# Performance work log

Hardware: AMD Instinct MI355X
Metric: run time of the kernel (lower is better)

Reference implementation:

```python
import jax, jax.numpy as jnp
import numpy as np

N_NODES = 65536
N_EDGES = 524288
N_LAYERS = 3
D = 128
ED = 32
BATCH = 64
NEG_SLOPE = 0.2


def setup_inputs() -> dict:
    key = jax.random.key(0)
    ks = jax.random.split(key, 10)
    w_scale = 1.0 / np.sqrt(D)
    return {
        "x": jax.random.normal(ks[0], (N_NODES, D), dtype=jnp.float32),
        "edge_index": jax.random.randint(ks[1], (2, N_EDGES), 0, N_NODES, dtype=jnp.int32),
        "edge_attr": jax.random.normal(ks[2], (N_EDGES, ED), dtype=jnp.float32),
        "Ws": jax.random.normal(ks[3], (N_LAYERS, D, D), dtype=jnp.float32) * w_scale,
        "att_src": jax.random.normal(ks[4], (N_LAYERS, D), dtype=jnp.float32) * w_scale,
        "att_dst": jax.random.normal(ks[5], (N_LAYERS, D), dtype=jnp.float32) * w_scale,
        "W_edge": jax.random.normal(ks[6], (N_LAYERS, ED, D), dtype=jnp.float32) * (1.0 / np.sqrt(ED)),
        "att_edge": jax.random.normal(ks[7], (N_LAYERS, D), dtype=jnp.float32) * w_scale,
        "bias": jnp.zeros((N_LAYERS, D), dtype=jnp.float32),
        "batch_size": BATCH,
    }


def _gat_layer(x, src, dst, ea, W, a_s, a_d, We, a_e, b, n):
    # PyG GATConv, heads=1, concat=True, flow source_to_target.
    h = x @ W                                      # [N, D]
    al = (h @ a_s)[src] + (h @ a_d)[dst] + (ea @ We) @ a_e   # [E]
    al = jax.nn.leaky_relu(al, NEG_SLOPE)
    # segment softmax over destination-node neighborhoods
    m = jax.ops.segment_max(al, dst, num_segments=n)
    ex = jnp.exp(al - m[dst])
    den = jax.ops.segment_sum(ex, dst, num_segments=n)
    w = ex / den[dst]                              # [E]
    out = jax.ops.segment_sum(w[:, None] * h[src], dst, num_segments=n)
    return out + b


def reference(x, edge_index, edge_attr, Ws, att_src, att_dst, W_edge, att_edge, bias, batch_size):
    n = x.shape[0]
    # add_self_loops with fill_value='mean': self-loop edge_attr is the mean of
    # incoming edge features per destination node (zero if no incoming edges).
    loop = jnp.arange(n, dtype=edge_index.dtype)
    src = jnp.concatenate([edge_index[0], loop])
    dst = jnp.concatenate([edge_index[1], loop])
    cnt = jax.ops.segment_sum(jnp.ones((edge_attr.shape[0],), edge_attr.dtype), edge_index[1], num_segments=n)
    fill = jax.ops.segment_sum(edge_attr, edge_index[1], num_segments=n) / jnp.maximum(cnt, 1.0)[:, None]
    ea = jnp.concatenate([edge_attr, fill], axis=0)

    h = x
    for l in range(Ws.shape[0]):
        h = jax.nn.gelu(
            _gat_layer(h, src, dst, ea, Ws[l], att_src[l], att_dst[l], W_edge[l], att_edge[l], bias[l], n),
            approximate=False,
        )
        # dropout p=0.2 is identity in eval mode
    return h.reshape(batch_size, n // batch_size, -1)
```

## Files before the change

### kernel.cpp

```cpp
#include <hip/hip_runtime.h>
#include <math.h>

#define NN 65536
#define NE 524288
#define D 128
#define ED 32
#define NEG_SLOPE 0.2f

typedef short bf16x8 __attribute__((ext_vector_type(8)));
typedef float f32x4 __attribute__((ext_vector_type(4)));
typedef unsigned short ushort_t;

__device__ __forceinline__ float leaky(float x) { return x > 0.f ? x : NEG_SLOPE * x; }
__device__ __forceinline__ float gelu_exact(float x) {
    return 0.5f * x * (1.f + erff(x * 0.70710678118654752440f));
}
__device__ __forceinline__ unsigned short bf16_rne(float x) {
    unsigned u = __float_as_uint(x);
    return (unsigned short)((u + 0x7FFFu + ((u >> 16) & 1u)) >> 16);
}
__device__ __forceinline__ void unpack8(int4 r, float* f) {
    unsigned u0 = (unsigned)r.x, u1 = (unsigned)r.y, u2 = (unsigned)r.z, u3 = (unsigned)r.w;
    f[0] = __uint_as_float(u0 << 16); f[1] = __uint_as_float(u0 & 0xFFFF0000u);
    f[2] = __uint_as_float(u1 << 16); f[3] = __uint_as_float(u1 & 0xFFFF0000u);
    f[4] = __uint_as_float(u2 << 16); f[5] = __uint_as_float(u2 & 0xFFFF0000u);
    f[6] = __uint_as_float(u3 << 16); f[7] = __uint_as_float(u3 & 0xFFFF0000u);
}


__global__ void k_wvec(const float* __restrict__ We, const float* __restrict__ ae, float* __restrict__ wvec) {
    int t = threadIdx.x;
    if (t < 3 * ED) {
        int l = t / ED, k = t % ED;
        const float* w = We + (long)(l * ED + k) * D;
        const float* a = ae + (long)l * D;
        float s = 0.f;
        #pragma unroll
        for (int i = 0; i < D; ++i) s += w[i] * a[i];
        wvec[t] = s;
    }
}

__global__ void k_ale_hist(const float* __restrict__ ea, const float* __restrict__ wvec,
                           const int* __restrict__ dstArr, int* __restrict__ deg,
                           float* __restrict__ ale0, float* __restrict__ ale1,
                           float* __restrict__ ale2) {
    int e = blockIdx.x * 256 + threadIdx.x;
    atomicAdd(&deg[dstArr[e]], 1);
    const float4* row = (const float4*)(ea + (long)e * ED);
    const float4* w0 = (const float4*)(wvec);
    const float4* w1 = (const float4*)(wvec + ED);
    const float4* w2 = (const float4*)(wvec + 2 * ED);
    float s0 = 0.f, s1 = 0.f, s2 = 0.f;
    #pragma unroll
    for (int i = 0; i < ED / 4; ++i) {
        float4 v = row[i];
        float4 a = w0[i], b = w1[i], c = w2[i];
        s0 += v.x * a.x + v.y * a.y + v.z * a.z + v.w * a.w;
        s1 += v.x * b.x + v.y * b.y + v.z * b.z + v.w * b.w;
        s2 += v.x * c.x + v.y * c.y + v.z * c.z + v.w * c.w;
    }
    ale0[e] = s0;
    ale1[e] = s1;
    ale2[e] = s2;
}

__global__ void k_scan1(const int* __restrict__ deg, int* __restrict__ rp, int* __restrict__ bsum) {
    __shared__ int s[256];
    int t = threadIdx.x;
    int i = blockIdx.x * 256 + t;
    int v = deg[i];
    s[t] = v;
    __syncthreads();
    #pragma unroll
    for (int off = 1; off < 256; off <<= 1) {
        int x = (t >= off) ? s[t - off] : 0;
        __syncthreads();
        s[t] += x;
        __syncthreads();
    }
    rp[i] = s[t] - v;
    if (t == 255) bsum[blockIdx.x] = s[t];
}

__global__ void k_scan2(const int* __restrict__ bsum, int* __restrict__ bscan, int* __restrict__ rp) {
    __shared__ int s[256];
    int t = threadIdx.x;
    int v = bsum[t];
    s[t] = v;
    __syncthreads();
    #pragma unroll
    for (int off = 1; off < 256; off <<= 1) {
        int x = (t >= off) ? s[t - off] : 0;
        __syncthreads();
        s[t] += x;
        __syncthreads();
    }
    bscan[t] = s[t] - v;
    if (t == 255) rp[NN] = s[t];
}

__global__ void k_scan3(int* __restrict__ rp, const int* __restrict__ bscan, int* __restrict__ cursor) {
    int i = blockIdx.x * 256 + threadIdx.x;
    int v = rp[i] + bscan[blockIdx.x];
    rp[i] = v;
    cursor[i] = v;
}

__global__ void k_scatter4(const int* __restrict__ srcArr, const int* __restrict__ dstArr,
                           int* __restrict__ cursor, const float* __restrict__ ale0,
                           const float* __restrict__ ale1, const float* __restrict__ ale2,
                           int4* __restrict__ edata) {
    int base = blockIdx.x * 1024 + threadIdx.x;
    int e[4], d[4], p[4];
    #pragma unroll
    for (int i = 0; i < 4; ++i) e[i] = base + 256 * i;
    #pragma unroll
    for (int i = 0; i < 4; ++i) d[i] = dstArr[e[i]];
    #pragma unroll
    for (int i = 0; i < 4; ++i) p[i] = atomicAdd(&cursor[d[i]], 1);
    #pragma unroll
    for (int i = 0; i < 4; ++i) {
        edata[p[i]] = make_int4(srcArr[e[i]], __float_as_int(ale0[e[i]]),
                                __float_as_int(ale1[e[i]]), __float_as_int(ale2[e[i]]));
    }
}

__global__ void k_wpack(const float* __restrict__ Ws, short* __restrict__ Whp, short* __restrict__ Wlp) {
    int t = blockIdx.x * 256 + threadIdx.x;
    if (t >= 3 * 4 * 4 * 128) return;
    int n = t & 127;
    int q = (t >> 7) & 3;
    int ks = (t >> 9) & 3;
    int l = t >> 11;
    const float* w = Ws + (size_t)l * D * D;
    size_t obase = (size_t)l * D * D + ((size_t)((ks * 4 + q) * 128) + n) * 8;
    #pragma unroll
    for (int j = 0; j < 8; ++j) {
        float x = w[(size_t)(ks * 32 + q * 8 + j) * D + n];
        unsigned short hb = bf16_rne(x);
        float hf = __uint_as_float(((unsigned)hb) << 16);
        Whp[obase + j] = (short)hb;
        Wlp[obase + j] = (short)bf16_rne(x - hf);
    }
}

__global__ void k_splitx(const float* __restrict__ x, ushort_t* __restrict__ Hh,
                         ushort_t* __restrict__ Hl) {
    int i = blockIdx.x * 256 + threadIdx.x;
    float4 v = ((const float4*)x)[i];
    float xs[4] = {v.x, v.y, v.z, v.w};
    ushort4 h, l;
    ushort_t* hp = (ushort_t*)&h;
    ushort_t* lp = (ushort_t*)&l;
    #pragma unroll
    for (int j = 0; j < 4; ++j) {
        unsigned short hb = bf16_rne(xs[j]);
        float hf = __uint_as_float(((unsigned)hb) << 16);
        hp[j] = hb;
        lp[j] = bf16_rne(xs[j] - hf);
    }
    ((ushort4*)Hh)[i] = h;
    ((ushort4*)Hl)[i] = l;
}


__global__ __launch_bounds__(256) void k_gemm_mfma(const ushort_t* __restrict__ Ah,
        const ushort_t* __restrict__ Al,
        const short* __restrict__ Whp, const short* __restrict__ Wlp,
        const float* __restrict__ a_s, const float* __restrict__ a_d,
        ushort_t* __restrict__ Hb, float* __restrict__ als, float* __restrict__ ald) {
    __shared__ int4 BsH[1024];
    __shared__ int4 BsL[1024];
    int t = threadIdx.x;
    int wave = t >> 6, lane = t & 63;
    int l16 = lane & 15, q = lane >> 4;
    int rows_base = blockIdx.x * 128 + wave * 32;

    const int4* wh4 = (const int4*)Whp;
    const int4* wl4 = (const int4*)Wlp;
    const short* bsh = (const short*)BsH;
    const short* bsl = (const short*)BsL;

    f32x4 acc[2][8] = {};
    #pragma unroll
    for (int h2 = 0; h2 < 2; ++h2) {
        if (h2) __syncthreads();
        #pragma unroll
        for (int i = 0; i < 4; ++i) {
            BsH[t + 256 * i] = wh4[h2 * 1024 + t + 256 * i];
            BsL[t + 256 * i] = wl4[h2 * 1024 + t + 256 * i];
        }
        __syncthreads();
        #pragma unroll
        for (int kk = 0; kk < 2; ++kk) {
            int ks = h2 * 2 + kk;
            bf16x8 ah[2], alo[2];
            #pragma unroll
            for (int mt = 0; mt < 2; ++mt) {
                size_t abase = (size_t)(rows_base + mt * 16 + l16) * D + ks * 32 + q * 8;
                ah[mt]  = *(const bf16x8*)(Ah + abase);
                alo[mt] = *(const bf16x8*)(Al + abase);
            }
            #pragma unroll
            for (int nt = 0; nt < 8; ++nt) {
                int idx = (((kk * 4 + q) * 128) + nt * 16 + l16) * 8;
                bf16x8 bh = *(const bf16x8*)(bsh + idx);
                bf16x8 bl = *(const bf16x8*)(bsl + idx);
                #pragma unroll
                for (int mt = 0; mt < 2; ++mt) {
                    acc[mt][nt] = __builtin_amdgcn_mfma_f32_16x16x32_bf16(ah[mt], bh, acc[mt][nt], 0, 0, 0);
                    acc[mt][nt] = __builtin_amdgcn_mfma_f32_16x16x32_bf16(ah[mt], bl, acc[mt][nt], 0, 0, 0);
                    acc[mt][nt] = __builtin_amdgcn_mfma_f32_16x16x32_bf16(alo[mt], bh, acc[mt][nt], 0, 0, 0);
                }
            }
        }
    }

    float as_r[8], ad_r[8];
    #pragma unroll
    for (int nt = 0; nt < 8; ++nt) {
        int col = nt * 16 + l16;
        as_r[nt] = a_s[col];
        ad_r[nt] = a_d[col];
    }
    #pragma unroll
    for (int mt = 0; mt < 2; ++mt) {
        #pragma unroll
        for (int r = 0; r < 4; ++r) {
            int row = rows_base + mt * 16 + q * 4 + r;
            float ps = 0.f, pd = 0.f;
            #pragma unroll
            for (int nt = 0; nt < 8; ++nt) {
                float v = acc[mt][nt][r];
                ps += v * as_r[nt];
                pd += v * ad_r[nt];
                Hb[(size_t)row * D + nt * 16 + l16] = bf16_rne(v);
            }
            #pragma unroll
            for (int off = 8; off >= 1; off >>= 1) {
                ps += __shfl_xor(ps, off);
                pd += __shfl_xor(pd, off);
            }
            if (l16 == 0) {
                als[row] = ps;
                ald[row] = pd;
            }
        }
    }
}

__global__ __launch_bounds__(256) void k_aggr_fused(const ushort_t* __restrict__ hb,
        const float* __restrict__ als, const float* __restrict__ ald,
        const int4* __restrict__ edata, const int* __restrict__ rp,
        const float* __restrict__ bias, int lsel, float* __restrict__ out_f32,
        ushort_t* __restrict__ out_hi, ushort_t* __restrict__ out_lo) {
    int t = threadIdx.x;
    int lane = t & 63;
    int l16 = lane & 15;
    int qb = lane & 48;
    int n = blockIdx.x * 16 + (t >> 4);
    int s = rp[n], e = rp[n + 1];
    int deg = e - s;
    float aldd = ald[n];
    float alsn = als[n];
    float inv_deg = (deg > 0) ? 1.f / (float)deg : 0.f;

    int4 hvp = *(const int4*)(hb + (size_t)n * D + l16 * 8);
    float acc8[8];

    if (deg <= 16) {
        int sn0 = 0;
        float al0 = -1e30f, alev0 = 0.f;
        if (l16 < deg) {
            int4 ed = edata[s + l16];
            sn0 = ed.x;
            alev0 = __int_as_float((lsel == 0) ? ed.y : ((lsel == 1) ? ed.z : ed.w));
            al0 = leaky(als[sn0] + aldd + alev0);
        }
        float mm = al0, asum = alev0;
        #pragma unroll
        for (int off = 1; off < 16; off <<= 1) {
            mm = fmaxf(mm, __shfl_xor(mm, off));
            asum += __shfl_xor(asum, off);
        }
        float self_al = leaky(alsn + aldd + asum * inv_deg);
        mm = fmaxf(mm, self_al);
        float p0 = (l16 < deg) ? __expf(al0 - mm) : 0.f;
        float den = p0;
        #pragma unroll
        for (int off = 1; off < 16; off <<= 1) den += __shfl_xor(den, off);
        float es = __expf(self_al - mm);
        den += es;
        float inv = 1.f / den;
        float w0 = p0 * inv;
        float wself = es * inv;

        float fv[8];
        unpack8(hvp, fv);
        #pragma unroll
        for (int j = 0; j < 8; ++j) acc8[j] = wself * fv[j];

        int tt = 0;
        for (; tt + 4 <= deg; tt += 4) {
            int   sA = __shfl(sn0, qb + tt),     sB = __shfl(sn0, qb + tt + 1);
            int   sC = __shfl(sn0, qb + tt + 2), sD = __shfl(sn0, qb + tt + 3);
            float wA = __shfl(w0, qb + tt),      wB = __shfl(w0, qb + tt + 1);
            float wC = __shfl(w0, qb + tt + 2),  wD = __shfl(w0, qb + tt + 3);
            int4 rA = *(const int4*)(hb + (size_t)sA * D + l16 * 8);
            int4 rB = *(const int4*)(hb + (size_t)sB * D + l16 * 8);
            int4 rC = *(const int4*)(hb + (size_t)sC * D + l16 * 8);
            int4 rD = *(const int4*)(hb + (size_t)sD * D + l16 * 8);
            float fA[8], fB[8], fC[8], fD[8];
            unpack8(rA, fA); unpack8(rB, fB); unpack8(rC, fC); unpack8(rD, fD);
            #pragma unroll
            for (int j = 0; j < 8; ++j)
                acc8[j] += wA * fA[j] + wB * fB[j] + wC * fC[j] + wD * fD[j];
        }
        for (; tt < deg; ++tt) {
            int st = __shfl(sn0, qb + tt);
            float wt = __shfl(w0, qb + tt);
            int4 r = *(const int4*)(hb + (size_t)st * D + l16 * 8);
            float f[8];
            unpack8(r, f);
            #pragma unroll
            for (int j = 0; j < 8; ++j) acc8[j] += wt * f[j];
        }
    } else {
        float mm = -1e30f, asum = 0.f;
        for (int base = s; base < e; base += 16) {
            int j = base + l16;
            if (j < e) {
                int4 ed = edata[j];
                float alev = __int_as_float((lsel == 0) ? ed.y : ((lsel == 1) ? ed.z : ed.w));
                asum += alev;
                mm = fmaxf(mm, leaky(als[ed.x] + aldd + alev));
            }
        }
        #pragma unroll
        for (int off = 1; off < 16; off <<= 1) {
            mm = fmaxf(mm, __shfl_xor(mm, off));
            asum += __shfl_xor(asum, off);
        }
        float self_al = leaky(alsn + aldd + asum * inv_deg);
        mm = fmaxf(mm, self_al);
        float den = 0.f;
        for (int base = s; base < e; base += 16) {
            int j = base + l16;
            if (j < e) {
                int4 ed = edata[j];
                float alev = __int_as_float((lsel == 0) ? ed.y : ((lsel == 1) ? ed.z : ed.w));
                den += __expf(leaky(als[ed.x] + aldd + alev) - mm);
            }
        }
        #pragma unroll
        for (int off = 1; off < 16; off <<= 1) den += __shfl_xor(den, off);
        float es = __expf(self_al - mm);
        den += es;
        float inv = 1.f / den;
        float wself = es * inv;
        float fv[8];
        unpack8(hvp, fv);
        #pragma unroll
        for (int j = 0; j < 8; ++j) acc8[j] = wself * fv[j];
        for (int base = s; base < e; base += 16) {
            int cnt = min(e - base, 16);
            int sn = 0;
            float w = 0.f;
            if (l16 < cnt) {
                int4 ed = edata[base + l16];
                sn = ed.x;
                float alev = __int_as_float((lsel == 0) ? ed.y : ((lsel == 1) ? ed.z : ed.w));
                w = __expf(leaky(als[sn] + aldd + alev) - mm) * inv;
            }
            for (int tt = 0; tt < cnt; ++tt) {
                int st = __shfl(sn, qb + tt);
                float wt = __shfl(w, qb + tt);
                int4 r = *(const int4*)(hb + (size_t)st * D + l16 * 8);
                float f[8];
                unpack8(r, f);
                #pragma unroll
                for (int j = 0; j < 8; ++j) acc8[j] += wt * f[j];
            }
        }
    }

    const float4* b4 = (const float4*)(bias + l16 * 8);
    float4 b0 = b4[0], b1 = b4[1];
    float bb[8] = {b0.x, b0.y, b0.z, b0.w, b1.x, b1.y, b1.z, b1.w};
    float o[8];
    #pragma unroll
    for (int j = 0; j < 8; ++j) o[j] = gelu_exact(acc8[j] + bb[j]);

    if (out_f32) {
        float4* o4 = (float4*)(out_f32 + (size_t)n * D + l16 * 8);
        o4[0] = make_float4(o[0], o[1], o[2], o[3]);
        o4[1] = make_float4(o[4], o[5], o[6], o[7]);
    } else {
        ushort4 hi0, hi1, lo0, lo1;
        ushort_t* h0p = (ushort_t*)&hi0; ushort_t* h1p = (ushort_t*)&hi1;
        ushort_t* l0p = (ushort_t*)&lo0; ushort_t* l1p = (ushort_t*)&lo1;
        #pragma unroll
        for (int j = 0; j < 8; ++j) {
            unsigned short hb16 = bf16_rne(o[j]);
            float hf = __uint_as_float(((unsigned)hb16) << 16);
            unsigned short lb16 = bf16_rne(o[j] - hf);
            if (j < 4) { h0p[j] = hb16; l0p[j] = lb16; }
            else       { h1p[j - 4] = hb16; l1p[j - 4] = lb16; }
        }
        ushort4* oh = (ushort4*)(out_hi + (size_t)n * D + l16 * 8);
        ushort4* ol = (ushort4*)(out_lo + (size_t)n * D + l16 * 8);
        oh[0] = hi0; oh[1] = hi1;
        ol[0] = lo0; ol[1] = lo1;
    }
}


extern "C" void kernel_launch(void* const* d_in, const int* in_sizes, int n_in,
                              void* d_out, int out_size, void* d_ws, size_t ws_size,
                              hipStream_t stream) {
    (void)in_sizes; (void)n_in; (void)out_size; (void)ws_size;
    const float* x        = (const float*)d_in[0];
    const int*   eidx     = (const int*)d_in[1];
    const float* ea       = (const float*)d_in[2];
    const float* Ws       = (const float*)d_in[3];
    const float* att_src  = (const float*)d_in[4];
    const float* att_dst  = (const float*)d_in[5];
    const float* W_edge   = (const float*)d_in[6];
    const float* att_edge = (const float*)d_in[7];
    const float* bias     = (const float*)d_in[8];
    float* out = (float*)d_out;

    char* ws = (char*)d_ws;
    size_t off = 0;
    auto alloc = [&](size_t bytes) {
        void* p = ws + off;
        off += (bytes + 255) & ~(size_t)255;
        return p;
    };
    ushort_t* Hb   = (ushort_t*)alloc((size_t)NN * D * 2);
    ushort_t* Hh   = (ushort_t*)alloc((size_t)NN * D * 2);
    ushort_t* Hl   = (ushort_t*)alloc((size_t)NN * D * 2);
    float*    als  = (float*)alloc((size_t)NN * 4);
    float*    ald  = (float*)alloc((size_t)NN * 4);
    int4*     edata= (int4*)alloc((size_t)NE * 16);
    float*    ale0 = (float*)alloc((size_t)NE * 4);
    float*    ale1 = (float*)alloc((size_t)NE * 4);
    float*    ale2 = (float*)alloc((size_t)NE * 4);
    float*    wvec = (float*)alloc(3 * ED * 4);
    int*      deg  = (int*)alloc((size_t)NN * 4);
    int*      rp   = (int*)alloc((size_t)(NN + 4) * 4);
    int*      cursor = (int*)alloc((size_t)NN * 4);
    int*      bsum = (int*)alloc(256 * 4);
    int*      bscan= (int*)alloc(256 * 4);
    short*    Whp  = (short*)alloc((size_t)3 * D * D * 2);
    short*    Wlp  = (short*)alloc((size_t)3 * D * D * 2);

    const int* e_src = eidx;
    const int* e_dst = eidx + NE;

    hipMemsetAsync(deg, 0, (size_t)NN * 4, stream);
    k_wvec<<<1, 128, 0, stream>>>(W_edge, att_edge, wvec);
    k_ale_hist<<<NE / 256, 256, 0, stream>>>(ea, wvec, e_dst, deg, ale0, ale1, ale2);
    k_scan1<<<NN / 256, 256, 0, stream>>>(deg, rp, bsum);
    k_scan2<<<1, 256, 0, stream>>>(bsum, bscan, rp);
    k_scan3<<<NN / 256, 256, 0, stream>>>(rp, bscan, cursor);
    k_scatter4<<<NE / 1024, 256, 0, stream>>>(e_src, e_dst, cursor, ale0, ale1, ale2, edata);

    k_wpack<<<24, 256, 0, stream>>>(Ws, Whp, Wlp);
    k_splitx<<<(NN * D / 4) / 256, 256, 0, stream>>>(x, Hh, Hl);

    for (int l = 0; l < 3; ++l) {
        k_gemm_mfma<<<NN / 128, 256, 0, stream>>>(Hh, Hl, Whp + (size_t)l * D * D, Wlp + (size_t)l * D * D,
                                                  att_src + (size_t)l * D, att_dst + (size_t)l * D,
                                                  Hb, als, ald);
        bool last = (l == 2);
        k_aggr_fused<<<NN / 16, 256, 0, stream>>>(Hb, als, ald, edata, rp, bias + (size_t)l * D, l,
                                                  last ? out : nullptr, Hh, Hl);
    }
}
```

Measured before the change: 366.9 us.

## Fuse bf16 hi/lo split into GEMM and stage H output through swizzled LDS

Removes the separate split-x kernel and the hi/lo bf16 intermediate buffers. The GEMM now reads fp32 activations directly and splits them into hi/lo bf16 in registers, while the aggregation kernel writes fp32 for every layer. The MFMA operand order is swapped so each lane holds 4 consecutive output columns, which allows vectorized attention dot products with fewer shuffles. The bf16 H tile is staged through XOR-swizzled shared memory so global stores are coalesced 16-byte writes. In exchange, GEMM A-reads and aggregation writes both stay the same byte count as before, and the split arithmetic is redone inside the GEMM.

Result: faster. 352.2 us (-4.0%).

```diff
diff --git a/kernel.cpp b/kernel.cpp
--- a/kernel.cpp
+++ b/kernel.cpp
@@ -145,33 +145,12 @@
     }
 }
 
-__global__ void k_splitx(const float* __restrict__ x, ushort_t* __restrict__ Hh,
-                         ushort_t* __restrict__ Hl) {
-    int i = blockIdx.x * 256 + threadIdx.x;
-    float4 v = ((const float4*)x)[i];
-    float xs[4] = {v.x, v.y, v.z, v.w};
-    ushort4 h, l;
-    ushort_t* hp = (ushort_t*)&h;
-    ushort_t* lp = (ushort_t*)&l;
-    #pragma unroll
-    for (int j = 0; j < 4; ++j) {
-        unsigned short hb = bf16_rne(xs[j]);
-        float hf = __uint_as_float(((unsigned)hb) << 16);
-        hp[j] = hb;
-        lp[j] = bf16_rne(xs[j] - hf);
-    }
-    ((ushort4*)Hh)[i] = h;
-    ((ushort4*)Hl)[i] = l;
-}
-
-
-__global__ __launch_bounds__(256) void k_gemm_mfma(const ushort_t* __restrict__ Ah,
-        const ushort_t* __restrict__ Al,
+
+__global__ __launch_bounds__(256) void k_gemm_mfma(const float* __restrict__ A,
         const short* __restrict__ Whp, const short* __restrict__ Wlp,
         const float* __restrict__ a_s, const float* __restrict__ a_d,
         ushort_t* __restrict__ Hb, float* __restrict__ als, float* __restrict__ ald) {
-    __shared__ int4 BsH[1024];
-    __shared__ int4 BsL[1024];
+    __shared__ int4 Bs[2048];
     int t = threadIdx.x;
     int wave = t >> 6, lane = t & 63;
     int l16 = lane & 15, q = lane >> 4;
@@ -179,8 +158,8 @@
 
     const int4* wh4 = (const int4*)Whp;
     const int4* wl4 = (const int4*)Wlp;
-    const short* bsh = (const short*)BsH;
-    const short* bsl = (const short*)BsL;
+    const short* bsh = (const short*)Bs;
+    const short* bsl = (const short*)(Bs + 1024);
 
     f32x4 acc[2][8] = {};
     #pragma unroll
@@ -188,8 +167,8 @@
         if (h2) __syncthreads();
         #pragma unroll
         for (int i = 0; i < 4; ++i) {
-            BsH[t + 256 * i] = wh4[h2 * 1024 + t + 256 * i];
-            BsL[t + 256 * i] = wl4[h2 * 1024 + t + 256 * i];
+            Bs[t + 256 * i] = wh4[h2 * 1024 + t + 256 * i];
+            Bs[1024 + t + 256 * i] = wl4[h2 * 1024 + t + 256 * i];
         }
         __syncthreads();
         #pragma unroll
@@ -198,9 +177,17 @@
             bf16x8 ah[2], alo[2];
             #pragma unroll
             for (int mt = 0; mt < 2; ++mt) {
-                size_t abase = (size_t)(rows_base + mt * 16 + l16) * D + ks * 32 + q * 8;
-                ah[mt]  = *(const bf16x8*)(Ah + abase);
-                alo[mt] = *(const bf16x8*)(Al + abase);
+                const float* ap = A + (size_t)(rows_base + mt * 16 + l16) * D + ks * 32 + q * 8;
+                float4 v0 = *(const float4*)ap;
+                float4 v1 = *(const float4*)(ap + 4);
+                float f[8] = {v0.x, v0.y, v0.z, v0.w, v1.x, v1.y, v1.z, v1.w};
+                #pragma unroll
+                for (int j = 0; j < 8; ++j) {
+                    unsigned short hb = bf16_rne(f[j]);
+                    float hf = __uint_as_float(((unsigned)hb) << 16);
+                    ah[mt][j]  = (short)hb;
+                    alo[mt][j] = (short)bf16_rne(f[j] - hf);
+                }
             }
             #pragma unroll
             for (int nt = 0; nt < 8; ++nt) {
@@ -209,52 +196,76 @@
                 bf16x8 bl = *(const bf16x8*)(bsl + idx);
                 #pragma unroll
                 for (int mt = 0; mt < 2; ++mt) {
-                    acc[mt][nt] = __builtin_amdgcn_mfma_f32_16x16x32_bf16(ah[mt], bh, acc[mt][nt], 0, 0, 0);
-                    acc[mt][nt] = __builtin_amdgcn_mfma_f32_16x16x32_bf16(ah[mt], bl, acc[mt][nt], 0, 0, 0);
-                    acc[mt][nt] = __builtin_amdgcn_mfma_f32_16x16x32_bf16(alo[mt], bh, acc[mt][nt], 0, 0, 0);
+                    acc[mt][nt] = __builtin_amdgcn_mfma_f32_16x16x32_bf16(bh, ah[mt], acc[mt][nt], 0, 0, 0);
+                    acc[mt][nt] = __builtin_amdgcn_mfma_f32_16x16x32_bf16(bl, ah[mt], acc[mt][nt], 0, 0, 0);
+                    acc[mt][nt] = __builtin_amdgcn_mfma_f32_16x16x32_bf16(bh, alo[mt], acc[mt][nt], 0, 0, 0);
                 }
             }
         }
     }
 
-    float as_r[8], ad_r[8];
+
+    float av[8][4], dv[8][4];
     #pragma unroll
     for (int nt = 0; nt < 8; ++nt) {
-        int col = nt * 16 + l16;
-        as_r[nt] = a_s[col];
-        ad_r[nt] = a_d[col];
+        float4 a4 = *(const float4*)(a_s + nt * 16 + q * 4);
+        float4 d4 = *(const float4*)(a_d + nt * 16 + q * 4);
+        av[nt][0] = a4.x; av[nt][1] = a4.y; av[nt][2] = a4.z; av[nt][3] = a4.w;
+        dv[nt][0] = d4.x; dv[nt][1] = d4.y; dv[nt][2] = d4.z; dv[nt][3] = d4.w;
     }
     #pragma unroll
     for (int mt = 0; mt < 2; ++mt) {
-        #pragma unroll
-        for (int r = 0; r < 4; ++r) {
-            int row = rows_base + mt * 16 + q * 4 + r;
-            float ps = 0.f, pd = 0.f;
+        float ps = 0.f, pd = 0.f;
+        #pragma unroll
+        for (int nt = 0; nt < 8; ++nt) {
             #pragma unroll
-            for (int nt = 0; nt < 8; ++nt) {
+            for (int r = 0; r < 4; ++r) {
                 float v = acc[mt][nt][r];
-                ps += v * as_r[nt];
-                pd += v * ad_r[nt];
-                Hb[(size_t)row * D + nt * 16 + l16] = bf16_rne(v);
-            }
-            #pragma unroll
-            for (int off = 8; off >= 1; off >>= 1) {
-                ps += __shfl_xor(ps, off);
-                pd += __shfl_xor(pd, off);
-            }
-            if (l16 == 0) {
-                als[row] = ps;
-                ald[row] = pd;
-            }
-        }
+                ps += v * av[nt][r];
+                pd += v * dv[nt][r];
+            }
+        }
+        ps += __shfl_xor(ps, 16); pd += __shfl_xor(pd, 16);
+        ps += __shfl_xor(ps, 32); pd += __shfl_xor(pd, 32);
+        if (q == 0) {
+            als[rows_base + mt * 16 + l16] = ps;
+            ald[rows_base + mt * 16 + l16] = pd;
+        }
+    }
+
+    __syncthreads();
+    char* tb = (char*)Bs + wave * 8192;
+    #pragma unroll
+    for (int mt = 0; mt < 2; ++mt) {
+        int row = mt * 16 + l16;
+        unsigned key = (unsigned)(row & 7) << 4;
+        #pragma unroll
+        for (int nt = 0; nt < 8; ++nt) {
+            ushort4 pk;
+            pk.x = bf16_rne(acc[mt][nt][0]);
+            pk.y = bf16_rne(acc[mt][nt][1]);
+            pk.z = bf16_rne(acc[mt][nt][2]);
+            pk.w = bf16_rne(acc[mt][nt][3]);
+            unsigned byteoff = (unsigned)row * 256u + (unsigned)(nt * 16 + q * 4) * 2u;
+            *(ushort4*)(tb + (byteoff ^ key)) = pk;
+        }
+    }
+    __syncthreads();
+    #pragma unroll
+    for (int i = 0; i < 8; ++i) {
+        int m = lane + 64 * i;
+        unsigned row = (unsigned)m >> 4;
+        unsigned byteoff = (unsigned)m * 16u;
+        unsigned addr = byteoff ^ ((row & 7u) << 4);
+        int4 v = *(const int4*)(tb + addr);
+        *(int4*)((char*)Hb + (size_t)rows_base * 256 + (size_t)m * 16) = v;
     }
 }
 
 __global__ __launch_bounds__(256) void k_aggr_fused(const ushort_t* __restrict__ hb,
         const float* __restrict__ als, const float* __restrict__ ald,
         const int4* __restrict__ edata, const int* __restrict__ rp,
-        const float* __restrict__ bias, int lsel, float* __restrict__ out_f32,
-        ushort_t* __restrict__ out_hi, ushort_t* __restrict__ out_lo) {
+        const float* __restrict__ bias, int lsel, float* __restrict__ out_f32) {
     int t = threadIdx.x;
     int lane = t & 63;
     int l16 = lane & 15;
@@ -392,27 +403,9 @@
     #pragma unroll
     for (int j = 0; j < 8; ++j) o[j] = gelu_exact(acc8[j] + bb[j]);
 
-    if (out_f32) {
-        float4* o4 = (float4*)(out_f32 + (size_t)n * D + l16 * 8);
-        o4[0] = make_float4(o[0], o[1], o[2], o[3]);
-        o4[1] = make_float4(o[4], o[5], o[6], o[7]);
-    } else {
-        ushort4 hi0, hi1, lo0, lo1;
-        ushort_t* h0p = (ushort_t*)&hi0; ushort_t* h1p = (ushort_t*)&hi1;
-        ushort_t* l0p = (ushort_t*)&lo0; ushort_t* l1p = (ushort_t*)&lo1;
-        #pragma unroll
-        for (int j = 0; j < 8; ++j) {
-            unsigned short hb16 = bf16_rne(o[j]);
-            float hf = __uint_as_float(((unsigned)hb16) << 16);
-            unsigned short lb16 = bf16_rne(o[j] - hf);
-            if (j < 4) { h0p[j] = hb16; l0p[j] = lb16; }
-            else       { h1p[j - 4] = hb16; l1p[j - 4] = lb16; }
-        }
-        ushort4* oh = (ushort4*)(out_hi + (size_t)n * D + l16 * 8);
-        ushort4* ol = (ushort4*)(out_lo + (size_t)n * D + l16 * 8);
-        oh[0] = hi0; oh[1] = hi1;
-        ol[0] = lo0; ol[1] = lo1;
-    }
+    float4* o4 = (float4*)(out_f32 + (size_t)n * D + l16 * 8);
+    o4[0] = make_float4(o[0], o[1], o[2], o[3]);
+    o4[1] = make_float4(o[4], o[5], o[6], o[7]);
 }
 
 
@@ -439,8 +432,7 @@
         return p;
     };
     ushort_t* Hb   = (ushort_t*)alloc((size_t)NN * D * 2);
-    ushort_t* Hh   = (ushort_t*)alloc((size_t)NN * D * 2);
-    ushort_t* Hl   = (ushort_t*)alloc((size_t)NN * D * 2);
+    float*    Hx   = (float*)alloc((size_t)NN * D * 4);
     float*    als  = (float*)alloc((size_t)NN * 4);
     float*    ald  = (float*)alloc((size_t)NN * 4);
     int4*     edata= (int4*)alloc((size_t)NE * 16);
@@ -468,14 +460,14 @@
     k_scatter4<<<NE / 1024, 256, 0, stream>>>(e_src, e_dst, cursor, ale0, ale1, ale2, edata);
 
     k_wpack<<<24, 256, 0, stream>>>(Ws, Whp, Wlp);
-    k_splitx<<<(NN * D / 4) / 256, 256, 0, stream>>>(x, Hh, Hl);
 
     for (int l = 0; l < 3; ++l) {
-        k_gemm_mfma<<<NN / 128, 256, 0, stream>>>(Hh, Hl, Whp + (size_t)l * D * D, Wlp + (size_t)l * D * D,
+        k_gemm_mfma<<<NN / 128, 256, 0, stream>>>(l == 0 ? x : Hx,
+                                                  Whp + (size_t)l * D * D, Wlp + (size_t)l * D * D,
                                                   att_src + (size_t)l * D, att_dst + (size_t)l * D,
                                                   Hb, als, ald);
         bool last = (l == 2);
         k_aggr_fused<<<NN / 16, 256, 0, stream>>>(Hb, als, ald, edata, rp, bias + (size_t)l * D, l,
-                                                  last ? out : nullptr, Hh, Hl);
-    }
-}
+                                                  last ? out : Hx);
+    }
+}
```
